# Performance work log

Hardware: AMD Instinct MI355X
Metric: run time of the kernel (lower is better)

## Reference

```python
import jax, jax.numpy as jnp
import numpy as np

INPUT_SIZE, HIDDEN_SIZE, OUTPUT_SIZE = 2, 512, 512
ALPHA = 0.1


def setup_inputs() -> dict:
    key = jax.random.key(0)
    ks = jax.random.split(key, 8)
    B, T = 256, 512
    inputs = jax.random.normal(ks[0], (B, T, INPUT_SIZE), dtype=jnp.float32)
    init_context = jax.random.normal(ks[1], (B, OUTPUT_SIZE), dtype=jnp.float32)
    # parameters (torch Linear convention: y = x @ W.T + b)
    W_in = jax.random.normal(ks[2], (HIDDEN_SIZE, INPUT_SIZE), dtype=jnp.float32) * (1.0 / np.sqrt(INPUT_SIZE + HIDDEN_SIZE))
    b_in = jnp.zeros((HIDDEN_SIZE,), dtype=jnp.float32)
    # orthogonal-ish recurrent weight via QR
    A = jax.random.normal(ks[3], (HIDDEN_SIZE, HIDDEN_SIZE), dtype=jnp.float32)
    W_rec, _ = jnp.linalg.qr(A)
    W_rec = W_rec.astype(jnp.float32)
    b_rec = jnp.zeros((HIDDEN_SIZE,), dtype=jnp.float32)
    W_out = jax.random.normal(ks[4], (OUTPUT_SIZE, HIDDEN_SIZE), dtype=jnp.float32) * (1.0 / np.sqrt(HIDDEN_SIZE + OUTPUT_SIZE))
    W_h_init = jax.random.normal(ks[5], (HIDDEN_SIZE, OUTPUT_SIZE), dtype=jnp.float32) * (1.0 / np.sqrt(HIDDEN_SIZE + OUTPUT_SIZE))
    return {"inputs": inputs, "init_context": init_context, "W_in": W_in, "b_in": b_in,
            "W_rec": W_rec, "b_rec": b_rec, "W_out": W_out, "W_h_init": W_h_init}


def reference(inputs, init_context, W_in, b_in, W_rec, b_rec, W_out, W_h_init):
    # inputs: (B, T, I); init_context: (B, O)
    h0 = init_context @ W_h_init.T  # (B, H)
    # precompute input projection for all timesteps: (B, T, H)
    x_proj = jnp.einsum('bti,hi->bth', inputs, W_in) + b_in

    def step(h, x_t):
        h_new = (1.0 - ALPHA) * h + ALPHA * jnp.tanh(x_t + h @ W_rec.T + b_rec)
        return h_new, h_new

    # scan over time: move T to leading axis
    _, hs = jax.lax.scan(step, h0, jnp.swapaxes(x_proj, 0, 1))  # hs: (T, B, H)
    hidden_states = jnp.swapaxes(hs, 0, 1)  # (B, T, H)
    outputs = jnp.einsum('bth,oh->bto', hidden_states, W_out)  # (B, T, O)
    return hidden_states, outputs
```

## Files before the change

### kernel.cpp

```cpp
#include <hip/hip_runtime.h>

typedef __bf16 bf16x8 __attribute__((ext_vector_type(8)));
typedef float f32x4 __attribute__((ext_vector_type(4)));
typedef unsigned int u32x4 __attribute__((ext_vector_type(4)));

union UQ { uint4 q; u32x4 p; bf16x8 v; __bf16 b[8]; unsigned long long d[2]; };

__device__ __forceinline__ unsigned short f2bf(float x){
  union { float f; unsigned u; } c; c.f = x;
  return (unsigned short)((c.u + 0x7fffu + ((c.u >> 16) & 1u)) >> 16);
}

__global__ void pack_kernel(const float* __restrict__ W, uint4* __restrict__ dst){
  int tid  = blockIdx.x * 512 + threadIdx.x;
  int lane = tid & 63;
  int kt   = (tid >> 6) & 15;
  int ntl  = tid >> 10;
  int row  = ntl * 16 + (lane & 15);
  int k0   = kt * 32 + ((lane >> 4) << 3);
  const float* s = &W[row * 512 + k0];
  unsigned a0 = f2bf(s[0]) | ((unsigned)f2bf(s[1]) << 16);
  unsigned a1 = f2bf(s[2]) | ((unsigned)f2bf(s[3]) << 16);
  unsigned a2 = f2bf(s[4]) | ((unsigned)f2bf(s[5]) << 16);
  unsigned a3 = f2bf(s[6]) | ((unsigned)f2bf(s[7]) << 16);
  dst[tid] = (uint4){a0, a1, a2, a3};
}

__global__ void h0_kernel(const float* __restrict__ init, const float* __restrict__ Whi,
                          float* __restrict__ h0, unsigned short* __restrict__ hb0){
  int b = blockIdx.x, n = threadIdx.x;
  __shared__ float ic[512];
  ic[n] = init[b * 512 + n];
  __syncthreads();
  const float4* wr = (const float4*)&Whi[n * 512];
  float s = 0.f;
  #pragma unroll 8
  for (int o = 0; o < 128; o++){
    float4 w = wr[o];
    s += w.x * ic[4*o] + w.y * ic[4*o+1] + w.z * ic[4*o+2] + w.w * ic[4*o+3];
  }
  h0[b * 512 + n] = s;
  hb0[b * 512 + n] = f2bf(s);
}

__global__ __launch_bounds__(512, 2)
void rnn_kernel(const float* __restrict__ inputs, const float* __restrict__ W_in,
                const float* __restrict__ b_in, const float* __restrict__ b_rec,
                const uint4* __restrict__ wfrag, const float* __restrict__ h0,
                const unsigned short* __restrict__ hb0, float* __restrict__ hidden){
  const int m = blockIdx.x;
  const int g16 = m << 4;
  const int tid = threadIdx.x, w = tid >> 6, lane = tid & 63;
  const int col = lane & 15, quad = lane >> 4;
  const int nbase = w << 6;
  const int swc = (col & 7) << 3;

  __shared__ unsigned short hbuf[16 * 512];
  __shared__ uint4 wlds[8][16][64];

  UQ u[32];
  #pragma unroll
  for (int kt = 0; kt < 8; kt++)
    #pragma unroll
    for (int nt = 0; nt < 4; nt++){
      const uint4* src = &wfrag[(((w << 2) + nt) * 16 + kt) * 64 + lane];
      asm volatile("global_load_dwordx4 %0, %1, off"
                   : "=v"(u[kt * 4 + nt].p) : "v"(src) : "memory");
    }
  asm volatile("s_waitcnt vmcnt(0)" ::: "memory");
  #pragma unroll
  for (int j = 0; j < 32; j++)
    asm volatile("" : "+v"(u[j].d[0]), "+v"(u[j].d[1]));

  #pragma unroll
  for (int kt = 8; kt < 12; kt++)
    #pragma unroll
    for (int nt = 0; nt < 4; nt++)
      wlds[w][(kt - 8) * 4 + nt][lane] = wfrag[(((w << 2) + nt) * 16 + kt) * 64 + lane];

  UQ uaug[4];
  #pragma unroll
  for (int nt = 0; nt < 4; nt++){
    uaug[nt].d[0] = 0; uaug[nt].d[1] = 0;
    if (quad == 0){
      int n = nbase + nt * 16 + col;
      uaug[nt].b[0] = (__bf16)W_in[2 * n];
      uaug[nt].b[1] = (__bf16)W_in[2 * n + 1];
      uaug[nt].b[2] = (__bf16)(b_in[n] + b_rec[n]);
    }
  }

  float h[16];
  #pragma unroll
  for (int nt = 0; nt < 4; nt++){
    float4 h4 = *(const float4*)&h0[(g16 + col) * 512 + nbase + nt * 16 + (quad << 2)];
    h[nt*4+0] = h4.x; h[nt*4+1] = h4.y; h[nt*4+2] = h4.z; h[nt*4+3] = h4.w;
  }

  {
    int b = tid >> 5, n0 = (tid & 31) << 4;
    const uint4* s4 = (const uint4*)&hb0[(g16 + b) * 512 + n0];
    uint4 v0 = s4[0], v1 = s4[1];
    int sw = (b & 7) << 3;
    *(uint4*)&hbuf[(b << 9) + (n0 ^ sw)]       = v0;
    *(uint4*)&hbuf[(b << 9) + ((n0 + 8) ^ sw)] = v1;
  }
  __syncthreads();

  unsigned long long wsp = (unsigned long long)wfrag;
  const float2* xsrc = (const float2*)&inputs[((size_t)(g16 + col)) << 10];

#define ISSUE(b4) { const int kt_ = 12 + (b4);                                    \
    _Pragma("unroll")                                                             \
    for (int nt_ = 0; nt_ < 4; nt_++)                                             \
      sv[(b4)*4 + nt_].q = ws[(((w << 2) + nt_) * 16 + kt_) * 64 + lane]; }

#define HREAD(kt_) *(const uint4*)&hbuf[(col << 9) + ((((kt_) << 5) + (quad << 3)) ^ swc)]

  for (int t = 0; t < 512; t++){
    asm volatile("" : "+s"(wsp));
    const uint4* ws = (const uint4*)wsp;

    UQ baug; baug.d[0] = 0; baug.d[1] = 0;
    float2 xv = xsrc[t];
    if (quad == 0){
      baug.b[0] = (__bf16)xv.x; baug.b[1] = (__bf16)xv.y; baug.b[2] = (__bf16)1.0f;
    }

    f32x4 acc[4];
    #pragma unroll
    for (int nt = 0; nt < 4; nt++)
      acc[nt] = __builtin_amdgcn_mfma_f32_16x16x32_bf16(uaug[nt].v, baug.v,
                                                        (f32x4){0.f,0.f,0.f,0.f}, 0, 0, 0);

    UQ sv[16];
    ISSUE(0);

    UQ bh[16];
    #pragma unroll
    for (int kt = 0; kt < 16; kt++)
      bh[kt].q = HREAD(kt);

    #pragma unroll
    for (int kt = 0; kt < 8; kt++){
      #pragma unroll
      for (int nt = 0; nt < 4; nt++)
        acc[nt] = __builtin_amdgcn_mfma_f32_16x16x32_bf16(u[kt*4+nt].v, bh[kt].v, acc[nt], 0, 0, 0);
      if (kt == 0) ISSUE(1);
      if (kt == 2) ISSUE(2);
      if (kt == 4) ISSUE(3);
    }
    #pragma unroll
    for (int kt = 8; kt < 12; kt++){
      #pragma unroll
      for (int nt = 0; nt < 4; nt++){
        UQ a; a.q = wlds[w][(kt - 8) * 4 + nt][lane];
        acc[nt] = __builtin_amdgcn_mfma_f32_16x16x32_bf16(a.v, bh[kt].v, acc[nt], 0, 0, 0);
      }
    }
    #pragma unroll
    for (int kt = 12; kt < 16; kt++){
      #pragma unroll
      for (int nt = 0; nt < 4; nt++)
        acc[nt] = __builtin_amdgcn_mfma_f32_16x16x32_bf16(sv[(kt-12)*4+nt].v, bh[kt].v, acc[nt], 0, 0, 0);
    }

    __syncthreads();

    #pragma unroll
    for (int nt = 0; nt < 4; nt++){
      UQ hw; hw.d[0] = 0; hw.d[1] = 0;
      #pragma unroll
      for (int r = 0; r < 4; r++){
        float z  = acc[nt][r];
        float e  = __expf(2.0f * z);
        float rc = __builtin_amdgcn_rcpf(e + 1.0f);
        float hn = fmaf(0.9f, h[nt*4+r], 0.1f) - 0.2f * rc;
        h[nt*4+r] = hn;
        hw.b[r] = (__bf16)hn;
      }
      *(unsigned long long*)&hbuf[(col << 9) + ((nbase + (nt << 4) + (quad << 2)) ^ swc)] = hw.d[0];
      *(float4*)&hidden[((size_t)(g16 + col) * 512 + t) * 512 + nbase + (nt << 4) + (quad << 2)] =
          (float4){h[nt*4+0], h[nt*4+1], h[nt*4+2], h[nt*4+3]};
    }
    __syncthreads();
  }
#undef ISSUE
#undef HREAD
}

__global__ __launch_bounds__(512, 2)
void out_gemm(const float* __restrict__ hidden, const uint4* __restrict__ wofrag,
              float* __restrict__ outp){
  const int tid  = threadIdx.x;
  const int w    = tid >> 6;
  const int lane = tid & 63;
  const int col  = lane & 15;
  const int quad = lane >> 4;
  const int ms   = w >> 1;
  const int nh   = w & 1;
  const int m0   = blockIdx.x << 7;

  __shared__ unsigned short albf[128 * 32];
  __shared__ uint4 wq[32][64];

  f32x4 acc[2][16];
  #pragma unroll
  for (int mt = 0; mt < 2; mt++)
    #pragma unroll
    for (int nt = 0; nt < 16; nt++) acc[mt][nt] = (f32x4){0.f, 0.f, 0.f, 0.f};

  for (int kt = 0; kt < 16; kt++){
    #pragma unroll
    for (int i = 0; i < 2; i++){
      int r  = (tid >> 3) + (i << 6);
      int c4 = (tid & 7) << 2;
      float4 v = *(const float4*)&hidden[(m0 + r) * 512 + (kt << 5) + c4];
      unsigned lo = f2bf(v.x) | ((unsigned)f2bf(v.y) << 16);
      unsigned hi = f2bf(v.z) | ((unsigned)f2bf(v.w) << 16);
      int byteoff = (r << 6) + ((c4 << 1) ^ (((r >> 1) & 3) << 4));
      *(uint2*)((char*)albf + byteoff) = (uint2){lo, hi};
    }
    #pragma unroll
    for (int j = 0; j < 4; j++){
      int idx = (j << 9) + tid;
      wq[idx >> 6][idx & 63] = wofrag[(((idx >> 6) << 4) + kt) * 64 + (idx & 63)];
    }
    __syncthreads();

    bf16x8 af[2];
    #pragma unroll
    for (int mt = 0; mt < 2; mt++){
      int rl = (ms << 5) + (mt << 4) + col;
      int byteoff = (rl << 6) + ((quad << 4) ^ (((rl >> 1) & 3) << 4));
      af[mt] = *(const bf16x8*)((const char*)albf + byteoff);
    }

    #pragma unroll
    for (int nt = 0; nt < 16; nt++){
      UQ u; u.q = wq[(nh << 4) + nt][lane];
      acc[0][nt] = __builtin_amdgcn_mfma_f32_16x16x32_bf16(af[0], u.v, acc[0][nt], 0, 0, 0);
      acc[1][nt] = __builtin_amdgcn_mfma_f32_16x16x32_bf16(af[1], u.v, acc[1][nt], 0, 0, 0);
    }
    __syncthreads();
  }

  #pragma unroll
  for (int mt = 0; mt < 2; mt++)
    #pragma unroll
    for (int nt = 0; nt < 16; nt++)
      #pragma unroll
      for (int r = 0; r < 4; r++)
        outp[(m0 + (ms << 5) + (mt << 4) + (quad << 2) + r) * 512
             + (nh << 8) + (nt << 4) + col] = acc[mt][nt][r];
}

extern "C" void kernel_launch(void* const* d_in, const int* in_sizes, int n_in,
                              void* d_out, int out_size, void* d_ws, size_t ws_size,
                              hipStream_t stream){
  const float* inputs  = (const float*)d_in[0];
  const float* initc   = (const float*)d_in[1];
  const float* W_in    = (const float*)d_in[2];
  const float* b_in    = (const float*)d_in[3];
  const float* W_rec   = (const float*)d_in[4];
  const float* b_rec   = (const float*)d_in[5];
  const float* W_out   = (const float*)d_in[6];
  const float* W_hi    = (const float*)d_in[7];

  float* hidden  = (float*)d_out;
  float* outputs = hidden + (size_t)67108864;

  char* ws = (char*)d_ws;
  uint4*          wrec_f = (uint4*)ws;
  uint4*          wout_f = (uint4*)(ws + (512 << 10));
  float*          h0     = (float*)(ws + (1024 << 10));
  unsigned short* hb0    = (unsigned short*)(ws + (1536 << 10));

  pack_kernel<<<64, 512, 0, stream>>>(W_rec, wrec_f);
  pack_kernel<<<64, 512, 0, stream>>>(W_out, wout_f);
  h0_kernel<<<256, 512, 0, stream>>>(initc, W_hi, h0, hb0);
  rnn_kernel<<<16, 512, 0, stream>>>(inputs, W_in, b_in, b_rec, wrec_f, h0, hb0, hidden);
  out_gemm<<<1024, 512, 0, stream>>>(hidden, wout_f, outputs);
}
```

Before: 1.699 ms.

## Keep more recurrent weight tiles in registers and stream h fragments per k-step

Moves the register-resident share of W_rec from 8 to 10 k-tiles per wave, shifts the LDS-resident window to k-tiles 10-13, and leaves only 2 k-tiles reloaded from global memory each timestep instead of 4. The 16 h-fragment LDS reads that were all hoisted up front are now read one per k-step, which frees VGPRs for the extra weight tiles. The aim is less per-step global weight traffic on the serial critical path, at the cost of LDS read latency that is less hidden and higher register pressure. The output store index is also widened to size_t.

```diff
diff --git a/kernel.cpp b/kernel.cpp
--- a/kernel.cpp
+++ b/kernel.cpp
@@ -58,25 +58,33 @@
   __shared__ unsigned short hbuf[16 * 512];
   __shared__ uint4 wlds[8][16][64];
 
-  UQ u[32];
-  #pragma unroll
-  for (int kt = 0; kt < 8; kt++)
-    #pragma unroll
-    for (int nt = 0; nt < 4; nt++){
-      const uint4* src = &wfrag[(((w << 2) + nt) * 16 + kt) * 64 + lane];
-      asm volatile("global_load_dwordx4 %0, %1, off"
-                   : "=v"(u[kt * 4 + nt].p) : "v"(src) : "memory");
-    }
-  asm volatile("s_waitcnt vmcnt(0)" ::: "memory");
-  #pragma unroll
-  for (int j = 0; j < 32; j++)
-    asm volatile("" : "+v"(u[j].d[0]), "+v"(u[j].d[1]));
-
-  #pragma unroll
-  for (int kt = 8; kt < 12; kt++)
+  UQ u[40];
+  #pragma unroll
+  for (int kb = 0; kb < 5; kb++){
+    #pragma unroll
+    for (int kk = 0; kk < 2; kk++)
+      #pragma unroll
+      for (int nt = 0; nt < 4; nt++){
+        const int j = (kb * 2 + kk) * 4 + nt;
+        const uint4* src = &wfrag[(((w << 2) + nt) * 16 + (kb * 2 + kk)) * 64 + lane];
+        asm volatile("global_load_dwordx4 %0, %1, off"
+                     : "=v"(u[j].p) : "v"(src) : "memory");
+      }
+    asm volatile("s_waitcnt vmcnt(0)" ::: "memory");
+    #pragma unroll
+    for (int kk = 0; kk < 2; kk++)
+      #pragma unroll
+      for (int nt = 0; nt < 4; nt++){
+        const int j = (kb * 2 + kk) * 4 + nt;
+        asm volatile("" : "+v"(u[j].d[0]), "+v"(u[j].d[1]));
+      }
+  }
+
+  #pragma unroll
+  for (int kt = 10; kt < 14; kt++)
     #pragma unroll
     for (int nt = 0; nt < 4; nt++)
-      wlds[w][(kt - 8) * 4 + nt][lane] = wfrag[(((w << 2) + nt) * 16 + kt) * 64 + lane];
+      wlds[w][(kt - 10) * 4 + nt][lane] = wfrag[(((w << 2) + nt) * 16 + kt) * 64 + lane];
 
   UQ uaug[4];
   #pragma unroll
@@ -110,10 +118,10 @@
   unsigned long long wsp = (unsigned long long)wfrag;
   const float2* xsrc = (const float2*)&inputs[((size_t)(g16 + col)) << 10];
 
-#define ISSUE(b4) { const int kt_ = 12 + (b4);                                    \
+#define ISSUE(b1) { const int kt_ = 14 + (b1);                                    \
     _Pragma("unroll")                                                             \
     for (int nt_ = 0; nt_ < 4; nt_++)                                             \
-      sv[(b4)*4 + nt_].q = ws[(((w << 2) + nt_) * 16 + kt_) * 64 + lane]; }
+      sv[(b1)*4 + nt_].q = ws[(((w << 2) + nt_) * 16 + kt_) * 64 + lane]; }
 
 #define HREAD(kt_) *(const uint4*)&hbuf[(col << 9) + ((((kt_) << 5) + (quad << 3)) ^ swc)]
 
@@ -133,36 +141,31 @@
       acc[nt] = __builtin_amdgcn_mfma_f32_16x16x32_bf16(uaug[nt].v, baug.v,
                                                         (f32x4){0.f,0.f,0.f,0.f}, 0, 0, 0);
 
-    UQ sv[16];
+    UQ sv[8];
     ISSUE(0);
-
-    UQ bh[16];
-    #pragma unroll
-    for (int kt = 0; kt < 16; kt++)
-      bh[kt].q = HREAD(kt);
-
-    #pragma unroll
-    for (int kt = 0; kt < 8; kt++){
+    #pragma unroll
+    for (int kt = 0; kt < 10; kt++){
+      UQ bfr; bfr.q = HREAD(kt);
       #pragma unroll
       for (int nt = 0; nt < 4; nt++)
-        acc[nt] = __builtin_amdgcn_mfma_f32_16x16x32_bf16(u[kt*4+nt].v, bh[kt].v, acc[nt], 0, 0, 0);
-      if (kt == 0) ISSUE(1);
-      if (kt == 2) ISSUE(2);
-      if (kt == 4) ISSUE(3);
-    }
-    #pragma unroll
-    for (int kt = 8; kt < 12; kt++){
+        acc[nt] = __builtin_amdgcn_mfma_f32_16x16x32_bf16(u[kt*4+nt].v, bfr.v, acc[nt], 0, 0, 0);
+      if (kt == 2) ISSUE(1);
+    }
+    #pragma unroll
+    for (int kt = 10; kt < 14; kt++){
+      UQ bfr; bfr.q = HREAD(kt);
       #pragma unroll
       for (int nt = 0; nt < 4; nt++){
-        UQ a; a.q = wlds[w][(kt - 8) * 4 + nt][lane];
-        acc[nt] = __builtin_amdgcn_mfma_f32_16x16x32_bf16(a.v, bh[kt].v, acc[nt], 0, 0, 0);
-      }
-    }
-    #pragma unroll
-    for (int kt = 12; kt < 16; kt++){
+        UQ a; a.q = wlds[w][(kt - 10) * 4 + nt][lane];
+        acc[nt] = __builtin_amdgcn_mfma_f32_16x16x32_bf16(a.v, bfr.v, acc[nt], 0, 0, 0);
+      }
+    }
+    #pragma unroll
+    for (int kt = 14; kt < 16; kt++){
+      UQ bfr; bfr.q = HREAD(kt);
       #pragma unroll
       for (int nt = 0; nt < 4; nt++)
-        acc[nt] = __builtin_amdgcn_mfma_f32_16x16x32_bf16(sv[(kt-12)*4+nt].v, bh[kt].v, acc[nt], 0, 0, 0);
+        acc[nt] = __builtin_amdgcn_mfma_f32_16x16x32_bf16(sv[(kt-14)*4+nt].v, bfr.v, acc[nt], 0, 0, 0);
     }
 
     __syncthreads();
@@ -251,7 +254,7 @@
     for (int nt = 0; nt < 16; nt++)
       #pragma unroll
       for (int r = 0; r < 4; r++)
-        outp[(m0 + (ms << 5) + (mt << 4) + (quad << 2) + r) * 512
+        outp[(size_t)(m0 + (ms << 5) + (mt << 4) + (quad << 2) + r) * 512
              + (nh << 8) + (nt << 4) + col] = acc[mt][nt][r];
 }
 
```

Measured after the change: 2.105 ms. 1.24x slower.

## Fuse recurrent scan and output GEMM into one kernel with progress flags

Applied to the files above, without the earlier changes.

Merges the RNN recurrence and the output projection GEMM into a single launch. The first 16 blocks run the recurrence and publish per-group progress every 64 timesteps, while the remaining blocks spin on those flags and compute output tiles as soon as their hidden rows are ready. This overlaps the output GEMM with the serial scan instead of running it afterward. It relies on the recurrent blocks being scheduled before or alongside the spinning consumers, or it could deadlock, and it raises LDS use to force one block per CU.

```diff
diff --git a/kernel.cpp b/kernel.cpp
--- a/kernel.cpp
+++ b/kernel.cpp
@@ -9,6 +9,10 @@
 __device__ __forceinline__ unsigned short f2bf(float x){
   union { float f; unsigned u; } c; c.f = x;
   return (unsigned short)((c.u + 0x7fffu + ((c.u >> 16) & 1u)) >> 16);
+}
+
+__global__ void zero_flags(int* __restrict__ p){
+  p[threadIdx.x] = 0;
 }
 
 __global__ void pack_kernel(const float* __restrict__ W, uint4* __restrict__ dst){
@@ -43,216 +47,233 @@
   hb0[b * 512 + n] = f2bf(s);
 }
 
-__global__ __launch_bounds__(512, 2)
-void rnn_kernel(const float* __restrict__ inputs, const float* __restrict__ W_in,
-                const float* __restrict__ b_in, const float* __restrict__ b_rec,
-                const uint4* __restrict__ wfrag, const float* __restrict__ h0,
-                const unsigned short* __restrict__ hb0, float* __restrict__ hidden){
-  const int m = blockIdx.x;
-  const int g16 = m << 4;
+__global__ __launch_bounds__(512, 1)
+void rnn_gemm(const float* __restrict__ inputs, const float* __restrict__ W_in,
+              const float* __restrict__ b_in, const float* __restrict__ b_rec,
+              const uint4* __restrict__ wfrag, const uint4* __restrict__ wofrag,
+              const float* __restrict__ h0, const unsigned short* __restrict__ hb0,
+              int* __restrict__ progress, float* __restrict__ hidden,
+              float* __restrict__ outp){
+  __shared__ char smem[147456];
+  const int bid = blockIdx.x;
   const int tid = threadIdx.x, w = tid >> 6, lane = tid & 63;
   const int col = lane & 15, quad = lane >> 4;
-  const int nbase = w << 6;
-  const int swc = (col & 7) << 3;
-
-  __shared__ unsigned short hbuf[16 * 512];
-  __shared__ uint4 wlds[8][16][64];
-
-  UQ u[32];
-  #pragma unroll
-  for (int kt = 0; kt < 8; kt++)
+
+  if (bid < 16){
+    const int m = bid;
+    const int g16 = m << 4;
+    const int nbase = w << 6;
+    const int swc = (col & 7) << 3;
+    unsigned short* hbuf = (unsigned short*)smem;
+    uint4* wlds = (uint4*)(smem + 16384);
+
+    UQ u[32];
+    #pragma unroll
+    for (int kt = 0; kt < 8; kt++)
+      #pragma unroll
+      for (int nt = 0; nt < 4; nt++){
+        const uint4* src = &wfrag[(((w << 2) + nt) * 16 + kt) * 64 + lane];
+        asm volatile("global_load_dwordx4 %0, %1, off"
+                     : "=v"(u[kt * 4 + nt].p) : "v"(src) : "memory");
+      }
+    asm volatile("s_waitcnt vmcnt(0)" ::: "memory");
+    #pragma unroll
+    for (int j = 0; j < 32; j++)
+      asm volatile("" : "+v"(u[j].d[0]), "+v"(u[j].d[1]));
+
+    #pragma unroll
+    for (int kt = 8; kt < 12; kt++)
+      #pragma unroll
+      for (int nt = 0; nt < 4; nt++)
+        wlds[(w * 16 + (kt - 8) * 4 + nt) * 64 + lane] =
+            wfrag[(((w << 2) + nt) * 16 + kt) * 64 + lane];
+
+    UQ uaug[4];
     #pragma unroll
     for (int nt = 0; nt < 4; nt++){
-      const uint4* src = &wfrag[(((w << 2) + nt) * 16 + kt) * 64 + lane];
-      asm volatile("global_load_dwordx4 %0, %1, off"
-                   : "=v"(u[kt * 4 + nt].p) : "v"(src) : "memory");
-    }
-  asm volatile("s_waitcnt vmcnt(0)" ::: "memory");
-  #pragma unroll
-  for (int j = 0; j < 32; j++)
-    asm volatile("" : "+v"(u[j].d[0]), "+v"(u[j].d[1]));
-
-  #pragma unroll
-  for (int kt = 8; kt < 12; kt++)
-    #pragma unroll
-    for (int nt = 0; nt < 4; nt++)
-      wlds[w][(kt - 8) * 4 + nt][lane] = wfrag[(((w << 2) + nt) * 16 + kt) * 64 + lane];
-
-  UQ uaug[4];
-  #pragma unroll
-  for (int nt = 0; nt < 4; nt++){
-    uaug[nt].d[0] = 0; uaug[nt].d[1] = 0;
-    if (quad == 0){
-      int n = nbase + nt * 16 + col;
-      uaug[nt].b[0] = (__bf16)W_in[2 * n];
-      uaug[nt].b[1] = (__bf16)W_in[2 * n + 1];
-      uaug[nt].b[2] = (__bf16)(b_in[n] + b_rec[n]);
-    }
-  }
-
-  float h[16];
-  #pragma unroll
-  for (int nt = 0; nt < 4; nt++){
-    float4 h4 = *(const float4*)&h0[(g16 + col) * 512 + nbase + nt * 16 + (quad << 2)];
-    h[nt*4+0] = h4.x; h[nt*4+1] = h4.y; h[nt*4+2] = h4.z; h[nt*4+3] = h4.w;
-  }
-
-  {
-    int b = tid >> 5, n0 = (tid & 31) << 4;
-    const uint4* s4 = (const uint4*)&hb0[(g16 + b) * 512 + n0];
-    uint4 v0 = s4[0], v1 = s4[1];
-    int sw = (b & 7) << 3;
-    *(uint4*)&hbuf[(b << 9) + (n0 ^ sw)]       = v0;
-    *(uint4*)&hbuf[(b << 9) + ((n0 + 8) ^ sw)] = v1;
-  }
-  __syncthreads();
-
-  unsigned long long wsp = (unsigned long long)wfrag;
-  const float2* xsrc = (const float2*)&inputs[((size_t)(g16 + col)) << 10];
-
-#define ISSUE(b4) { const int kt_ = 12 + (b4);                                    \
+      uaug[nt].d[0] = 0; uaug[nt].d[1] = 0;
+      if (quad == 0){
+        int n = nbase + nt * 16 + col;
+        uaug[nt].b[0] = (__bf16)W_in[2 * n];
+        uaug[nt].b[1] = (__bf16)W_in[2 * n + 1];
+        uaug[nt].b[2] = (__bf16)(b_in[n] + b_rec[n]);
+      }
+    }
+
+    float h[16];
+    #pragma unroll
+    for (int nt = 0; nt < 4; nt++){
+      float4 h4 = *(const float4*)&h0[(g16 + col) * 512 + nbase + nt * 16 + (quad << 2)];
+      h[nt*4+0] = h4.x; h[nt*4+1] = h4.y; h[nt*4+2] = h4.z; h[nt*4+3] = h4.w;
+    }
+
+    {
+      int b = tid >> 5, n0 = (tid & 31) << 4;
+      const uint4* s4 = (const uint4*)&hb0[(g16 + b) * 512 + n0];
+      uint4 v0 = s4[0], v1 = s4[1];
+      int sw = (b & 7) << 3;
+      *(uint4*)&hbuf[(b << 9) + (n0 ^ sw)]       = v0;
+      *(uint4*)&hbuf[(b << 9) + ((n0 + 8) ^ sw)] = v1;
+    }
+    __syncthreads();
+
+    unsigned long long wsp = (unsigned long long)wfrag;
+    const float2* xsrc = (const float2*)&inputs[((size_t)(g16 + col)) << 10];
+
+#define ISSUE(b1) { const int kt_ = 12 + (b1);                                    \
     _Pragma("unroll")                                                             \
     for (int nt_ = 0; nt_ < 4; nt_++)                                             \
-      sv[(b4)*4 + nt_].q = ws[(((w << 2) + nt_) * 16 + kt_) * 64 + lane]; }
+      sv[(b1)*4 + nt_].q = ws[(((w << 2) + nt_) * 16 + kt_) * 64 + lane]; }
 
 #define HREAD(kt_) *(const uint4*)&hbuf[(col << 9) + ((((kt_) << 5) + (quad << 3)) ^ swc)]
 
-  for (int t = 0; t < 512; t++){
-    asm volatile("" : "+s"(wsp));
-    const uint4* ws = (const uint4*)wsp;
-
-    UQ baug; baug.d[0] = 0; baug.d[1] = 0;
-    float2 xv = xsrc[t];
-    if (quad == 0){
-      baug.b[0] = (__bf16)xv.x; baug.b[1] = (__bf16)xv.y; baug.b[2] = (__bf16)1.0f;
-    }
-
-    f32x4 acc[4];
-    #pragma unroll
-    for (int nt = 0; nt < 4; nt++)
-      acc[nt] = __builtin_amdgcn_mfma_f32_16x16x32_bf16(uaug[nt].v, baug.v,
-                                                        (f32x4){0.f,0.f,0.f,0.f}, 0, 0, 0);
-
-    UQ sv[16];
-    ISSUE(0);
-
-    UQ bh[16];
-    #pragma unroll
-    for (int kt = 0; kt < 16; kt++)
-      bh[kt].q = HREAD(kt);
-
-    #pragma unroll
-    for (int kt = 0; kt < 8; kt++){
+    for (int t = 0; t < 512; t++){
+      asm volatile("" : "+s"(wsp));
+      const uint4* ws = (const uint4*)wsp;
+
+      UQ baug; baug.d[0] = 0; baug.d[1] = 0;
+      float2 xv = xsrc[t];
+      if (quad == 0){
+        baug.b[0] = (__bf16)xv.x; baug.b[1] = (__bf16)xv.y; baug.b[2] = (__bf16)1.0f;
+      }
+
+      f32x4 acc[4];
       #pragma unroll
       for (int nt = 0; nt < 4; nt++)
-        acc[nt] = __builtin_amdgcn_mfma_f32_16x16x32_bf16(u[kt*4+nt].v, bh[kt].v, acc[nt], 0, 0, 0);
-      if (kt == 0) ISSUE(1);
-      if (kt == 2) ISSUE(2);
-      if (kt == 4) ISSUE(3);
-    }
-    #pragma unroll
-    for (int kt = 8; kt < 12; kt++){
+        acc[nt] = __builtin_amdgcn_mfma_f32_16x16x32_bf16(uaug[nt].v, baug.v,
+                                                          (f32x4){0.f,0.f,0.f,0.f}, 0, 0, 0);
+
+      UQ sv[16];
+      ISSUE(0);
+      UQ bh[16];
+      #pragma unroll
+      for (int kt = 0; kt < 16; kt++)
+        bh[kt].q = HREAD(kt);
+
+      #pragma unroll
+      for (int kt = 0; kt < 8; kt++){
+        #pragma unroll
+        for (int nt = 0; nt < 4; nt++)
+          acc[nt] = __builtin_amdgcn_mfma_f32_16x16x32_bf16(u[kt*4+nt].v, bh[kt].v, acc[nt], 0, 0, 0);
+        if (kt == 0) ISSUE(1);
+        if (kt == 2) ISSUE(2);
+        if (kt == 4) ISSUE(3);
+      }
+      #pragma unroll
+      for (int kt = 8; kt < 12; kt++){
+        #pragma unroll
+        for (int nt = 0; nt < 4; nt++){
+          UQ a; a.q = wlds[(w * 16 + (kt - 8) * 4 + nt) * 64 + lane];
+          acc[nt] = __builtin_amdgcn_mfma_f32_16x16x32_bf16(a.v, bh[kt].v, acc[nt], 0, 0, 0);
+        }
+      }
+      #pragma unroll
+      for (int kt = 12; kt < 16; kt++){
+        #pragma unroll
+        for (int nt = 0; nt < 4; nt++)
+          acc[nt] = __builtin_amdgcn_mfma_f32_16x16x32_bf16(sv[(kt-12)*4+nt].v, bh[kt].v, acc[nt], 0, 0, 0);
+      }
+
+      __syncthreads();
+
       #pragma unroll
       for (int nt = 0; nt < 4; nt++){
-        UQ a; a.q = wlds[w][(kt - 8) * 4 + nt][lane];
-        acc[nt] = __builtin_amdgcn_mfma_f32_16x16x32_bf16(a.v, bh[kt].v, acc[nt], 0, 0, 0);
-      }
-    }
-    #pragma unroll
-    for (int kt = 12; kt < 16; kt++){
-      #pragma unroll
-      for (int nt = 0; nt < 4; nt++)
-        acc[nt] = __builtin_amdgcn_mfma_f32_16x16x32_bf16(sv[(kt-12)*4+nt].v, bh[kt].v, acc[nt], 0, 0, 0);
-    }
-
-    __syncthreads();
-
-    #pragma unroll
-    for (int nt = 0; nt < 4; nt++){
-      UQ hw; hw.d[0] = 0; hw.d[1] = 0;
-      #pragma unroll
-      for (int r = 0; r < 4; r++){
-        float z  = acc[nt][r];
-        float e  = __expf(2.0f * z);
-        float rc = __builtin_amdgcn_rcpf(e + 1.0f);
-        float hn = fmaf(0.9f, h[nt*4+r], 0.1f) - 0.2f * rc;
-        h[nt*4+r] = hn;
-        hw.b[r] = (__bf16)hn;
-      }
-      *(unsigned long long*)&hbuf[(col << 9) + ((nbase + (nt << 4) + (quad << 2)) ^ swc)] = hw.d[0];
-      *(float4*)&hidden[((size_t)(g16 + col) * 512 + t) * 512 + nbase + (nt << 4) + (quad << 2)] =
-          (float4){h[nt*4+0], h[nt*4+1], h[nt*4+2], h[nt*4+3]};
-    }
-    __syncthreads();
-  }
+        UQ hw; hw.d[0] = 0; hw.d[1] = 0;
+        #pragma unroll
+        for (int r = 0; r < 4; r++){
+          float z  = acc[nt][r];
+          float e  = __expf(2.0f * z);
+          float rc = __builtin_amdgcn_rcpf(e + 1.0f);
+          float hn = fmaf(0.9f, h[nt*4+r], 0.1f) - 0.2f * rc;
+          h[nt*4+r] = hn;
+          hw.b[r] = (__bf16)hn;
+        }
+        *(unsigned long long*)&hbuf[(col << 9) + ((nbase + (nt << 4) + (quad << 2)) ^ swc)] = hw.d[0];
+        *(float4*)&hidden[((size_t)(g16 + col) * 512 + t) * 512 + nbase + (nt << 4) + (quad << 2)] =
+            (float4){h[nt*4+0], h[nt*4+1], h[nt*4+2], h[nt*4+3]};
+      }
+      __syncthreads();
+
+      if (((t + 1) & 63) == 0){
+        asm volatile("s_waitcnt vmcnt(0)" ::: "memory");
+        __syncthreads();
+        if (tid == 0){
+          __builtin_amdgcn_fence(__ATOMIC_RELEASE, "agent");
+          __hip_atomic_store(&progress[m], t + 1, __ATOMIC_RELAXED, __HIP_MEMORY_SCOPE_AGENT);
+        }
+      }
+    }
 #undef ISSUE
 #undef HREAD
-}
-
-__global__ __launch_bounds__(512, 2)
-void out_gemm(const float* __restrict__ hidden, const uint4* __restrict__ wofrag,
-              float* __restrict__ outp){
-  const int tid  = threadIdx.x;
-  const int w    = tid >> 6;
-  const int lane = tid & 63;
-  const int col  = lane & 15;
-  const int quad = lane >> 4;
-  const int ms   = w >> 1;
-  const int nh   = w & 1;
-  const int m0   = blockIdx.x << 7;
-
-  __shared__ unsigned short albf[128 * 32];
-  __shared__ uint4 wq[32][64];
-
-  f32x4 acc[2][16];
-  #pragma unroll
-  for (int mt = 0; mt < 2; mt++)
-    #pragma unroll
-    for (int nt = 0; nt < 16; nt++) acc[mt][nt] = (f32x4){0.f, 0.f, 0.f, 0.f};
-
-  for (int kt = 0; kt < 16; kt++){
-    #pragma unroll
-    for (int i = 0; i < 2; i++){
-      int r  = (tid >> 3) + (i << 6);
-      int c4 = (tid & 7) << 2;
-      float4 v = *(const float4*)&hidden[(m0 + r) * 512 + (kt << 5) + c4];
-      unsigned lo = f2bf(v.x) | ((unsigned)f2bf(v.y) << 16);
-      unsigned hi = f2bf(v.z) | ((unsigned)f2bf(v.w) << 16);
-      int byteoff = (r << 6) + ((c4 << 1) ^ (((r >> 1) & 3) << 4));
-      *(uint2*)((char*)albf + byteoff) = (uint2){lo, hi};
-    }
-    #pragma unroll
-    for (int j = 0; j < 4; j++){
-      int idx = (j << 9) + tid;
-      wq[idx >> 6][idx & 63] = wofrag[(((idx >> 6) << 4) + kt) * 64 + (idx & 63)];
-    }
+  } else {
+    const int gid = bid - 16;
+    const int m0  = gid << 7;
+    const int grp = gid >> 6;
+    const int thr = (m0 & 511) + 128;
+    const int ms  = w >> 1;
+    const int nh  = w & 1;
+    unsigned short* albf = (unsigned short*)smem;
+    uint4* wq = (uint4*)(smem + 8192);
+
+    if (tid == 0)
+      while (__hip_atomic_load(&progress[grp], __ATOMIC_RELAXED,
+                               __HIP_MEMORY_SCOPE_AGENT) < thr) {}
     __syncthreads();
 
-    bf16x8 af[2];
-    #pragma unroll
-    for (int mt = 0; mt < 2; mt++){
-      int rl = (ms << 5) + (mt << 4) + col;
-      int byteoff = (rl << 6) + ((quad << 4) ^ (((rl >> 1) & 3) << 4));
-      af[mt] = *(const bf16x8*)((const char*)albf + byteoff);
-    }
-
-    #pragma unroll
-    for (int nt = 0; nt < 16; nt++){
-      UQ u; u.q = wq[(nh << 4) + nt][lane];
-      acc[0][nt] = __builtin_amdgcn_mfma_f32_16x16x32_bf16(af[0], u.v, acc[0][nt], 0, 0, 0);
-      acc[1][nt] = __builtin_amdgcn_mfma_f32_16x16x32_bf16(af[1], u.v, acc[1][nt], 0, 0, 0);
-    }
-    __syncthreads();
+    f32x4 acc[2][16];
+    #pragma unroll
+    for (int mt = 0; mt < 2; mt++)
+      #pragma unroll
+      for (int nt = 0; nt < 16; nt++) acc[mt][nt] = (f32x4){0.f, 0.f, 0.f, 0.f};
+
+    for (int kt = 0; kt < 16; kt++){
+      #pragma unroll
+      for (int i = 0; i < 2; i++){
+        int r  = (tid >> 3) + (i << 6);
+        int c4 = (tid & 7) << 2;
+        const unsigned long long* hp =
+            (const unsigned long long*)&hidden[(size_t)(m0 + r) * 512 + (kt << 5) + c4];
+        unsigned long long d0 = __hip_atomic_load(hp,     __ATOMIC_RELAXED, __HIP_MEMORY_SCOPE_AGENT);
+        unsigned long long d1 = __hip_atomic_load(hp + 1, __ATOMIC_RELAXED, __HIP_MEMORY_SCOPE_AGENT);
+        union { unsigned long long d[2]; float f[4]; } cv; cv.d[0] = d0; cv.d[1] = d1;
+        unsigned lo = f2bf(cv.f[0]) | ((unsigned)f2bf(cv.f[1]) << 16);
+        unsigned hi = f2bf(cv.f[2]) | ((unsigned)f2bf(cv.f[3]) << 16);
+        int byteoff = (r << 6) + ((c4 << 1) ^ (((r >> 1) & 3) << 4));
+        *(uint2*)(smem + byteoff) = (uint2){lo, hi};
+      }
+      #pragma unroll
+      for (int j = 0; j < 4; j++){
+        int idx = (j << 9) + tid;
+        wq[(idx >> 6) * 64 + (idx & 63)] = wofrag[(((idx >> 6) << 4) + kt) * 64 + (idx & 63)];
+      }
+      __syncthreads();
+
+      bf16x8 af[2];
+      #pragma unroll
+      for (int mt = 0; mt < 2; mt++){
+        int rl = (ms << 5) + (mt << 4) + col;
+        int byteoff = (rl << 6) + ((quad << 4) ^ (((rl >> 1) & 3) << 4));
+        af[mt] = *(const bf16x8*)((const char*)albf + byteoff);
+      }
+
+      #pragma unroll
+      for (int nt = 0; nt < 16; nt++){
+        UQ uu; uu.q = wq[((nh << 4) + nt) * 64 + lane];
+        acc[0][nt] = __builtin_amdgcn_mfma_f32_16x16x32_bf16(af[0], uu.v, acc[0][nt], 0, 0, 0);
+        acc[1][nt] = __builtin_amdgcn_mfma_f32_16x16x32_bf16(af[1], uu.v, acc[1][nt], 0, 0, 0);
+      }
+      __syncthreads();
+    }
+
+    #pragma unroll
+    for (int mt = 0; mt < 2; mt++)
+      #pragma unroll
+      for (int nt = 0; nt < 16; nt++)
+        #pragma unroll
+        for (int r = 0; r < 4; r++)
+          outp[(size_t)(m0 + (ms << 5) + (mt << 4) + (quad << 2) + r) * 512
+               + (nh << 8) + (nt << 4) + col] = acc[mt][nt][r];
   }
-
-  #pragma unroll
-  for (int mt = 0; mt < 2; mt++)
-    #pragma unroll
-    for (int nt = 0; nt < 16; nt++)
-      #pragma unroll
-      for (int r = 0; r < 4; r++)
-        outp[(m0 + (ms << 5) + (mt << 4) + (quad << 2) + r) * 512
-             + (nh << 8) + (nt << 4) + col] = acc[mt][nt][r];
 }
 
 extern "C" void kernel_launch(void* const* d_in, const int* in_sizes, int n_in,
@@ -271,14 +292,16 @@
   float* outputs = hidden + (size_t)67108864;
 
   char* ws = (char*)d_ws;
-  uint4*          wrec_f = (uint4*)ws;
-  uint4*          wout_f = (uint4*)(ws + (512 << 10));
-  float*          h0     = (float*)(ws + (1024 << 10));
-  unsigned short* hb0    = (unsigned short*)(ws + (1536 << 10));
-
+  uint4*          wrec_f  = (uint4*)ws;
+  uint4*          wout_f  = (uint4*)(ws + (512 << 10));
+  float*          h0      = (float*)(ws + (1024 << 10));
+  unsigned short* hb0     = (unsigned short*)(ws + (1536 << 10));
+  int*            progress= (int*)(ws + (1792 << 10));
+
+  zero_flags<<<1, 64, 0, stream>>>(progress);
   pack_kernel<<<64, 512, 0, stream>>>(W_rec, wrec_f);
   pack_kernel<<<64, 512, 0, stream>>>(W_out, wout_f);
   h0_kernel<<<256, 512, 0, stream>>>(initc, W_hi, h0, hb0);
-  rnn_kernel<<<16, 512, 0, stream>>>(inputs, W_in, b_in, b_rec, wrec_f, h0, hb0, hidden);
-  out_gemm<<<1024, 512, 0, stream>>>(hidden, wout_f, outputs);
-}
+  rnn_gemm<<<1040, 512, 0, stream>>>(inputs, W_in, b_in, b_rec, wrec_f, wout_f,
+                                     h0, hb0, progress, hidden, outputs);
+}
```

Measured after the change: 1.804 ms. +6.2%, slower.
